# Performance work log

Measured on AMD Instinct MI355X. Metric: run time of the kernel, lower is better.

Reference implementation:

```python
import jax, jax.numpy as jnp
import numpy as np

INPUT_DIM = 1024
LATENT_DIM = 256
NUM_EMB = 8192
BATCH = 8192


def setup_inputs() -> dict:
    key = jax.random.key(0)
    ks = jax.random.split(key, 6)
    x = jax.random.normal(ks[0], (BATCH, INPUT_DIM), dtype=jnp.float32)
    # torch nn.Linear stores weight as [out, in]
    enc_w = jax.random.normal(ks[1], (LATENT_DIM, INPUT_DIM), dtype=jnp.float32) / np.sqrt(INPUT_DIM)
    enc_b = jnp.zeros((LATENT_DIM,), dtype=jnp.float32)
    # embeddings initialized uniform(-1/K, 1/K) as in the module
    emb = jax.random.uniform(ks[2], (NUM_EMB, LATENT_DIM), dtype=jnp.float32,
                             minval=-1.0 / NUM_EMB, maxval=1.0 / NUM_EMB)
    dec_w = jax.random.normal(ks[3], (INPUT_DIM, LATENT_DIM), dtype=jnp.float32) / np.sqrt(LATENT_DIM)
    dec_b = jnp.zeros((INPUT_DIM,), dtype=jnp.float32)
    return {"x": x, "enc_w": enc_w, "enc_b": enc_b, "emb": emb,
            "dec_w": dec_w, "dec_b": dec_b}


def reference(x, enc_w, enc_b, emb, dec_w, dec_b):
    # encoder: z = x @ W_e^T + b_e  -> [B, D]
    z = x @ enc_w.T + enc_b
    # cosine distance to codebook: d = 1 - <z, e> / (||z|| ||e||)  -> [B, K]
    z_norm = jnp.linalg.norm(z, axis=1, keepdims=True)          # [B, 1]
    e_norm = jnp.linalg.norm(emb, axis=1)                        # [K]
    d = 1.0 - (z @ emb.T) / (z_norm * e_norm)
    idx = jnp.argmin(d, axis=1)                                  # [B]
    # one-hot @ codebook == direct gather of nearest code vectors
    z_q = jnp.take(emb, idx, axis=0)                             # [B, D]
    # straight-through: decoder input z + stop_grad(z_q - z)
    dec_in = z + jax.lax.stop_gradient(z_q - z)
    x_recon = dec_in @ dec_w.T + dec_b
    return (x_recon, z, z_q, idx.astype(jnp.int32))
```

## Files before the change

### kernel.cpp

```cpp
#include <hip/hip_runtime.h>
#include <math.h>

#define BATCH   8192
#define IN_DIM  1024
#define LAT     256
#define NEMB    8192

#define TAU 3.5e-3f

#define RESC_R 16

#define CSPLIT 16

typedef _Float16 f16x8 __attribute__((ext_vector_type(8)));
typedef _Float16 f16x4 __attribute__((ext_vector_type(4)));
typedef float f32x16_t __attribute__((ext_vector_type(16)));

typedef __attribute__((address_space(1))) const unsigned int gu32_t;
typedef __attribute__((address_space(3))) unsigned int lu32_t;

__device__ __forceinline__ unsigned int ford(float x) {
  unsigned int u = __float_as_uint(x);
  return (u & 0x80000000u) ? ~u : (u | 0x80000000u);
}
__device__ __forceinline__ float funord(unsigned int t) {
  unsigned int u = (t & 0x80000000u) ? (t & 0x7FFFFFFFu) : ~t;
  return __uint_as_float(u);
}

__global__ __launch_bounds__(256) void emb_norms(
    const float* __restrict__ emb, float* __restrict__ inv_norm) {
  int row = blockIdx.x * 4 + (threadIdx.x >> 6);
  int lane = threadIdx.x & 63;
  const float* p = emb + (size_t)row * LAT;
  float s = 0.f;
#pragma unroll
  for (int t = 0; t < 4; ++t) {
    float v = p[lane + 64 * t];
    s += v * v;
  }
#pragma unroll
  for (int off = 32; off; off >>= 1) s += __shfl_xor(s, off);
  if (lane == 0) inv_norm[row] = 1.0f / sqrtf(s);
}

__global__ __launch_bounds__(256) void split16(
    const float* __restrict__ src, const float* __restrict__ inv_norm,
    _Float16* __restrict__ dst, size_t lo_off, int KD, int write_lo) {
  int gw = (blockIdx.x * 256 + threadIdx.x) >> 6;
  int l = threadIdx.x & 63;
  int tile = gw / KD, kb = gw % KD;
  int row = tile * 32 + (l & 31);
  int k = kb * 16 + (l >> 5) * 8;
  const float* p = src + (size_t)row * (KD * 16) + k;
  float scale = inv_norm ? inv_norm[row] : 1.0f;
  f16x8 h, lo;
#pragma unroll
  for (int j = 0; j < 8; ++j) {
    float v = p[j] * scale;
    _Float16 hh = (_Float16)v;
    h[j] = hh;
    lo[j] = (_Float16)(v - (float)hh);
  }
  size_t o = ((size_t)gw * 64 + l) * 8;
  *(f16x8*)(dst + o) = h;
  if (write_lo) *(f16x8*)(dst + lo_off + o) = lo;
}

__global__ __launch_bounds__(256) void gemm16_frag(
    const _Float16* __restrict__ Afrag, size_t a_lo_off,
    const _Float16* __restrict__ Bfrag, size_t b_lo_off,
    const float* __restrict__ bias, float* __restrict__ C, int N, int K) {
  __shared__ char lds[32768];
  const int tid = threadIdx.x;
  const int l = tid & 63;
  const int w = tid >> 6;
  const int mt = w & 1, nt = w >> 1;
  const int rb = blockIdx.y * 64, cb = blockIdx.x * 64;
  const int KD = K >> 4;

  f32x16_t acc = (f32x16_t)0.0f;

  for (int s = 0; s < (K >> 6); ++s) {
#pragma unroll
    for (int i = 0; i < 8; ++i) {
      int c = i * 4 + w;
      int isB = c >> 4;
      int cc = c & 15;
      int t32 = cc >> 3, prec = (cc >> 2) & 1, ks = cc & 3;
      int tile = ((isB ? cb : rb) >> 5) + t32;
      int kb = s * 4 + ks;
      const _Float16* base = isB ? Bfrag : Afrag;
      size_t lo = isB ? b_lo_off : a_lo_off;
      const _Float16* src =
          base + (size_t)prec * lo + ((size_t)(tile * KD + kb) * 64 + l) * 8;
      __builtin_amdgcn_global_load_lds((gu32_t*)src,
                                       (lu32_t*)(lds + (c << 10) + l * 16),
                                       16, 0, 0);
    }
    __syncthreads();
#pragma unroll
    for (int ks = 0; ks < 4; ++ks) {
      f16x8 ah = *(const f16x8*)(lds + ((mt * 8 + ks) << 10) + l * 16);
      f16x8 al = *(const f16x8*)(lds + ((mt * 8 + 4 + ks) << 10) + l * 16);
      f16x8 bh = *(const f16x8*)(lds + 16384 + ((nt * 8 + ks) << 10) + l * 16);
      f16x8 bl = *(const f16x8*)(lds + 16384 + ((nt * 8 + 4 + ks) << 10) + l * 16);
      acc = __builtin_amdgcn_mfma_f32_32x32x16_f16(ah, bh, acc, 0, 0, 0);
      acc = __builtin_amdgcn_mfma_f32_32x32x16_f16(ah, bl, acc, 0, 0, 0);
      acc = __builtin_amdgcn_mfma_f32_32x32x16_f16(al, bh, acc, 0, 0, 0);
    }
    __syncthreads();
  }

  int col = cb + nt * 32 + (l & 31);
  float bv = bias[col];
#pragma unroll
  for (int r = 0; r < 16; ++r) {
    int row = rb + mt * 32 + (r & 3) + 8 * (r >> 2) + 4 * (l >> 5);
    C[(size_t)row * N + col] = acc[r] + bv;
  }
}

__global__ __launch_bounds__(256) void gemm16(
    const float* __restrict__ A, const _Float16* __restrict__ Bfrag,
    size_t b_lo_off, const float* __restrict__ bias, float* __restrict__ C,
    int M, int N, int K) {
  __shared__ char lds[32768];
  const int tid = threadIdx.x;
  const int l = tid & 63;
  const int w = tid >> 6;
  const int mt = w & 1, nt = w >> 1;
  const int rb = blockIdx.y * 64, cb = blockIdx.x * 64;
  const int KD = K >> 4;

  f32x16_t acc = (f32x16_t)0.0f;

  for (int s = 0; s < (K >> 6); ++s) {
#pragma unroll
    for (int i = 0; i < 4; ++i) {
      int c = i * 4 + w;
      int bnt = c >> 3, prec = (c >> 2) & 1, ks = c & 3;
      int tile = (cb >> 5) + bnt, ksg = s * 4 + ks;
      const _Float16* src = Bfrag + (size_t)prec * b_lo_off +
                            ((size_t)(tile * KD + ksg) * 64 + l) * 8;
      __builtin_amdgcn_global_load_lds((gu32_t*)src,
                                       (lu32_t*)(lds + 16384 + (c << 10) + l * 16),
                                       16, 0, 0);
    }
#pragma unroll
    for (int t = 0; t < 4; ++t) {
      int flat = t * 256 + tid;
      int r = flat >> 4, c4 = flat & 15;
      float4 v = *(const float4*)&A[(size_t)(rb + r) * K + s * 64 + 4 * c4];
      int kk = 4 * c4;
      int ks = kk >> 4, j = kk & 7;
      int lane2 = (r & 31) + 32 * ((kk >> 3) & 1);
      int mtt = r >> 5;
      f16x4 hv, lv;
      float vv[4] = {v.x, v.y, v.z, v.w};
#pragma unroll
      for (int e = 0; e < 4; ++e) {
        _Float16 h = (_Float16)vv[e];
        hv[e] = h;
        lv[e] = (_Float16)(vv[e] - (float)h);
      }
      int base = ((mtt * 8 + ks) << 10) + lane2 * 16 + j * 2;
      *(f16x4*)(lds + base) = hv;
      *(f16x4*)(lds + base + 4096) = lv;
    }
    __syncthreads();
#pragma unroll
    for (int ks = 0; ks < 4; ++ks) {
      f16x8 ah = *(const f16x8*)(lds + ((mt * 8 + ks) << 10) + l * 16);
      f16x8 al = *(const f16x8*)(lds + ((mt * 8 + 4 + ks) << 10) + l * 16);
      f16x8 bh = *(const f16x8*)(lds + 16384 + ((nt * 8 + ks) << 10) + l * 16);
      f16x8 bl = *(const f16x8*)(lds + 16384 + ((nt * 8 + 4 + ks) << 10) + l * 16);
      acc = __builtin_amdgcn_mfma_f32_32x32x16_f16(ah, bh, acc, 0, 0, 0);
      acc = __builtin_amdgcn_mfma_f32_32x32x16_f16(ah, bl, acc, 0, 0, 0);
      acc = __builtin_amdgcn_mfma_f32_32x32x16_f16(al, bh, acc, 0, 0, 0);
    }
    __syncthreads();
  }

  int col = cb + nt * 32 + (l & 31);
  float bv = bias[col];
#pragma unroll
  for (int r = 0; r < 16; ++r) {
    int row = rb + mt * 32 + (r & 3) + 8 * (r >> 2) + 4 * (l >> 5);
    C[(size_t)row * N + col] = acc[r] + bv;
  }
}

__global__ __launch_bounds__(256) void score_mfma(
    const _Float16* __restrict__ zfrag, const _Float16* __restrict__ efrag,
    unsigned long long* __restrict__ cand1, unsigned int* __restrict__ cand2) {
  __shared__ char lds[32768];
  const int tid = threadIdx.x;
  const int l = tid & 63;
  const int w = tid >> 6;
  const int csplit = blockIdx.x;
  const int rowgrp = blockIdx.y;

  f16x8 a[16];
  {
    const _Float16* ab =
        zfrag + (((size_t)(rowgrp * 4 + w) * 16) * 64 + l) * 8;
#pragma unroll
    for (int kf = 0; kf < 16; ++kf)
      a[kf] = *(const f16x8*)(ab + (size_t)kf * 512);
  }

  float b1[16], b2[16];
  int i1[16];
#pragma unroll
  for (int r = 0; r < 16; ++r) {
    b1[r] = -INFINITY;
    b2[r] = -INFINITY;
    i1[r] = 0;
  }

  const char* esrc = (const char*)efrag + (size_t)csplit * 262144 + tid * 16;
  char* ldst = lds + tid * 16;
  const char* ldsr = lds + l * 16;

#pragma unroll
  for (int i = 0; i < 4; ++i)
    __builtin_amdgcn_global_load_lds((gu32_t*)(esrc + i * 4096),
                                     (lu32_t*)(ldst + i * 4096), 16, 0, 0);

#pragma unroll 1
  for (int p = 0; p < 16; ++p) {
    asm volatile("s_waitcnt vmcnt(0)" ::: "memory");
    __builtin_amdgcn_s_barrier();
    __builtin_amdgcn_sched_barrier(0);

    if (p < 15) {
      const char* sb = esrc + (size_t)(p + 1) * 16384;
      char* db = ldst + ((p + 1) & 1) * 16384;
#pragma unroll
      for (int i = 0; i < 4; ++i)
        __builtin_amdgcn_global_load_lds((gu32_t*)(sb + i * 4096),
                                         (lu32_t*)(db + i * 4096), 16, 0, 0);
    }

    const char* bb = ldsr + (p & 1) * 16384;
    f32x16_t acc0 = (f32x16_t)0.0f;
    f32x16_t acc1 = (f32x16_t)0.0f;
#pragma unroll
    for (int kb = 0; kb < 16; kb += 2) {
      f16x8 bh0 = *(const f16x8*)(bb + (kb << 10));
      f16x8 bh1 = *(const f16x8*)(bb + ((kb + 1) << 10));
      acc0 = __builtin_amdgcn_mfma_f32_32x32x16_f16(a[kb], bh0, acc0, 0, 0, 0);
      acc1 = __builtin_amdgcn_mfma_f32_32x32x16_f16(a[kb + 1], bh1, acc1, 0, 0, 0);
    }

    const int col = csplit * 512 + p * 32 + (l & 31);
#pragma unroll
    for (int r = 0; r < 16; ++r) {
      float v = acc0[r] + acc1[r];
      float nb2 = __builtin_amdgcn_fmed3f(v, b1[r], b2[r]);
      if (v > b1[r]) i1[r] = col;
      b1[r] = fmaxf(b1[r], v);
      b2[r] = nb2;
    }
  }

#pragma unroll
  for (int r = 0; r < 16; ++r) {
    float v1 = b1[r], v2 = b2[r];
    int vi = i1[r];
#pragma unroll
    for (int m = 1; m < 32; m <<= 1) {
      float o1 = __shfl_xor(v1, m);
      int oi = __shfl_xor(vi, m);
      float o2 = __shfl_xor(v2, m);
      float n2v = fmaxf(fminf(v1, o1), fmaxf(v2, o2));
      if (o1 > v1 || (o1 == v1 && oi < vi)) {
        v1 = o1;
        vi = oi;
      }
      v2 = n2v;
    }
    if ((l & 31) == 0) {
      int row = rowgrp * 128 + w * 32 + (r & 3) + 8 * (r >> 2) + 4 * (l >> 5);
      cand1[(size_t)row * CSPLIT + csplit] =
          ((unsigned long long)ford(v1) << 32) |
          (unsigned long long)(unsigned int)(NEMB - 1 - vi);
      cand2[(size_t)row * CSPLIT + csplit] = ford(v2);
    }
  }
}

__global__ __launch_bounds__(256) void finalize1(
    const unsigned long long* __restrict__ cand1,
    const unsigned int* __restrict__ cand2, int* __restrict__ idxi,
    unsigned int* __restrict__ flags, unsigned int* __restrict__ flag_count,
    unsigned int* __restrict__ flag_list) {
  int row = blockIdx.x * 256 + threadIdx.x;
  unsigned long long best = 0;
  unsigned int second = 0;
  int bslot = 0;
#pragma unroll
  for (int s = 0; s < CSPLIT; ++s) {
    unsigned long long v = cand1[(size_t)row * CSPLIT + s];
    unsigned int vs = (unsigned int)(v >> 32);
    if (v > best) {
      second = (unsigned int)(best >> 32);
      best = v;
      bslot = s;
    } else if (vs > second) {
      second = vs;
    }
  }
  unsigned int r2 = cand2[(size_t)row * CSPLIT + bslot];
  if (r2 > second) second = r2;
  float s1 = funord((unsigned int)(best >> 32));
  float s2 = funord(second);
  int idx = NEMB - 1 - (int)(best & 0xFFFFFFFFull);
  idxi[row] = idx;
  unsigned int fl = ((s1 - s2) < TAU) ? 1u : 0u;
  flags[row] = fl;
  if (fl) {
    unsigned int p = atomicAdd(flag_count, 1u);
    flag_list[p] = row;
  }
}

__global__ __launch_bounds__(256) void rescore(
    const float* __restrict__ z, const float* __restrict__ emb,
    const float* __restrict__ inv_norm,
    const unsigned int* __restrict__ flag_list,
    const unsigned int* __restrict__ flag_count,
    unsigned long long* __restrict__ packed_rescore) {
  __shared__ float z_s[2][292];
  __shared__ unsigned long long red[64];
  const int tid = threadIdx.x;
  const int l = tid & 63;
  const int w = tid >> 6;
  const int cl = l & 7;
  const int p = l >> 3;
  const int code = w * 8 + cl;
  const int cbase = blockIdx.x * 32;
  const unsigned int rc = blockIdx.y;

  unsigned int cnt = *flag_count;
  if (2 * rc >= cnt) return;

  float4 e4[8];
  const float* ebase = emb + (size_t)(cbase + code) * 256 + p * 32;
#pragma unroll
  for (int j = 0; j < 8; ++j) e4[j] = *(const float4*)&ebase[4 * j];
  const float inv = inv_norm[cbase + code];
  const unsigned int lowbits = (unsigned int)(NEMB - 1 - (cbase + code));

  for (unsigned int f = 2 * rc; f < cnt; f += 2 * RESC_R) {
    int row0 = (int)flag_list[f];
    int row1 = (f + 1 < cnt) ? (int)flag_list[f + 1] : row0;
    __syncthreads();
    if (tid < 128) {
      int half = tid >> 6, t = tid & 63;
      int k0 = t * 4;
      int addr = k0 + 4 * (k0 >> 5);
      const float* zp = z + (size_t)(half ? row1 : row0) * 256 + k0;
      *(float4*)&z_s[half][addr] = *(const float4*)zp;
    }
    __syncthreads();
    float a0 = 0.f, a1 = 0.f;
#pragma unroll
    for (int j = 0; j < 8; ++j) {
      float4 z0 = *(const float4*)&z_s[0][p * 36 + 4 * j];
      float4 z1 = *(const float4*)&z_s[1][p * 36 + 4 * j];
      a0 += e4[j].x * z0.x + e4[j].y * z0.y + e4[j].z * z0.z + e4[j].w * z0.w;
      a1 += e4[j].x * z1.x + e4[j].y * z1.y + e4[j].z * z1.z + e4[j].w * z1.w;
    }
#pragma unroll
    for (int m = 8; m < 64; m <<= 1) {
      a0 += __shfl_xor(a0, m);
      a1 += __shfl_xor(a1, m);
    }
    if (l < 8)
      red[w * 8 + cl] = ((unsigned long long)ford(a0 * inv) << 32) | lowbits;
    else if (l < 16)
      red[32 + w * 8 + cl] = ((unsigned long long)ford(a1 * inv) << 32) | lowbits;
    __syncthreads();
    if (w == 0) {
      unsigned long long v = red[l];
#pragma unroll
      for (int m = 1; m < 32; m <<= 1) {
        unsigned long long o = __shfl_xor(v, m);
        if (o > v) v = o;
      }
      if (l == 0) atomicMax(&packed_rescore[row0], v);
      if (l == 32) atomicMax(&packed_rescore[row1], v);
    }
  }
}

__global__ __launch_bounds__(256) void gather_split(
    const int* __restrict__ idxi, const unsigned int* __restrict__ flags,
    const unsigned long long* __restrict__ packed_rescore,
    const float* __restrict__ emb, float* __restrict__ zq,
    float* __restrict__ idx_out, _Float16* __restrict__ zqfrag,
    size_t lo_off, int use_frag) {
  __shared__ float zrow[32][260];
  __shared__ int idxs[32];
  const int tid = threadIdx.x;
  const int tile = blockIdx.x;
  if (tid < 32) {
    int row = tile * 32 + tid;
    int idx = idxi[row];
    if (flags[row]) idx = NEMB - 1 - (int)(packed_rescore[row] & 0xFFFFFFFFull);
    idxs[tid] = idx;
    idx_out[row] = (float)idx;
  }
  __syncthreads();
#pragma unroll
  for (int t = 0; t < 8; ++t) {
    int flat = t * 256 + tid;
    int r = flat >> 6, c4 = flat & 63;
    float4 v = *(const float4*)&emb[(size_t)idxs[r] * 256 + 4 * c4];
    *(float4*)&zrow[r][4 * c4] = v;
    *(float4*)&zq[(size_t)(tile * 32 + r) * 256 + 4 * c4] = v;
  }
  if (use_frag) {
    __syncthreads();
#pragma unroll
    for (int t = 0; t < 4; ++t) {
      int flat = t * 256 + tid;
      int fb = flat >> 6, fl = flat & 63;
      int r = fl & 31, k0 = fb * 16 + (fl >> 5) * 8;
      float4 v0 = *(const float4*)&zrow[r][k0];
      float4 v1 = *(const float4*)&zrow[r][k0 + 4];
      float vv[8] = {v0.x, v0.y, v0.z, v0.w, v1.x, v1.y, v1.z, v1.w};
      f16x8 hv, lv;
#pragma unroll
      for (int j = 0; j < 8; ++j) {
        _Float16 h = (_Float16)vv[j];
        hv[j] = h;
        lv[j] = (_Float16)(vv[j] - (float)h);
      }
      size_t g = ((size_t)(tile * 16 + fb) * 64 + fl) * 8;
      *(f16x8*)(zqfrag + g) = hv;
      *(f16x8*)(zqfrag + lo_off + g) = lv;
    }
  }
}

extern "C" void kernel_launch(void* const* d_in, const int* in_sizes, int n_in,
                              void* d_out, int out_size, void* d_ws,
                              size_t ws_size, hipStream_t stream) {
  (void)in_sizes; (void)n_in; (void)out_size;
  const float* x     = (const float*)d_in[0];
  const float* enc_w = (const float*)d_in[1];
  const float* enc_b = (const float*)d_in[2];
  const float* emb   = (const float*)d_in[3];
  const float* dec_w = (const float*)d_in[4];
  const float* dec_b = (const float*)d_in[5];

  float* out     = (float*)d_out;
  float* x_recon = out;
  float* z_out   = x_recon + (size_t)BATCH * IN_DIM;
  float* zq_out  = z_out + (size_t)BATCH * LAT;
  float* idx_out = zq_out + (size_t)BATCH * LAT;

  char* ws = (char*)d_ws;
  float* inv_norm = (float*)ws;
  unsigned int* flags = (unsigned int*)(ws + 32768);
  int* idxi = (int*)(ws + 65536);
  unsigned int* flag_count = (unsigned int*)(ws + 98304);
  unsigned long long* packed_rescore =
      (unsigned long long*)(ws + 98432);
  unsigned int* flag_list = (unsigned int*)(ws + 163968);
  _Float16* wfrag  = (_Float16*)(ws + 1048576);
  _Float16* dwfrag = (_Float16*)(ws + 2097152);
  _Float16* efrag  = (_Float16*)(ws + 3145728);
  _Float16* zfrag  = (_Float16*)(ws + 7340032);
  unsigned long long* cand1 = (unsigned long long*)(ws + 11534336);
  unsigned int* cand2 = (unsigned int*)(ws + 12582912);
  _Float16* zqfrag = (_Float16*)(ws + 15728640);
  _Float16* xfrag  = (_Float16*)(ws + 24117248);

  const bool has_zq = ws_size >= 24117248ull;
  const bool has_x  = ws_size >= 57671680ull;

  hipMemsetAsync(ws + 98304, 0, 128 + 65536, stream);

  emb_norms<<<NEMB / 4, 256, 0, stream>>>(emb, inv_norm);
  split16<<<128, 256, 0, stream>>>(enc_w, (const float*)nullptr, wfrag,
                                   (size_t)LAT * IN_DIM, IN_DIM / 16, 1);
  split16<<<128, 256, 0, stream>>>(dec_w, (const float*)nullptr, dwfrag,
                                   (size_t)IN_DIM * LAT, LAT / 16, 1);
  split16<<<1024, 256, 0, stream>>>(emb, inv_norm, efrag, 0, LAT / 16, 0);

  if (has_x) {
    split16<<<4096, 256, 0, stream>>>(x, (const float*)nullptr, xfrag,
                                      (size_t)BATCH * IN_DIM, IN_DIM / 16, 1);
    gemm16_frag<<<dim3(LAT / 64, BATCH / 64), 256, 0, stream>>>(
        xfrag, (size_t)BATCH * IN_DIM, wfrag, (size_t)LAT * IN_DIM, enc_b,
        z_out, LAT, IN_DIM);
  } else {
    gemm16<<<dim3(LAT / 64, BATCH / 64), 256, 0, stream>>>(
        x, wfrag, (size_t)LAT * IN_DIM, enc_b, z_out, BATCH, LAT, IN_DIM);
  }

  split16<<<1024, 256, 0, stream>>>(z_out, (const float*)nullptr, zfrag,
                                    (size_t)BATCH * LAT, LAT / 16, 0);

  score_mfma<<<dim3(CSPLIT, 64), 256, 0, stream>>>(zfrag, efrag, cand1, cand2);

  finalize1<<<32, 256, 0, stream>>>(cand1, cand2, idxi, flags, flag_count,
                                    flag_list);
  rescore<<<dim3(256, RESC_R), 256, 0, stream>>>(
      z_out, emb, inv_norm, flag_list, flag_count, packed_rescore);

  gather_split<<<BATCH / 32, 256, 0, stream>>>(
      idxi, flags, packed_rescore, emb, zq_out, idx_out,
      has_zq ? zqfrag : (_Float16*)nullptr, (size_t)BATCH * LAT,
      has_zq ? 1 : 0);

  if (has_zq) {
    gemm16_frag<<<dim3(IN_DIM / 64, BATCH / 64), 256, 0, stream>>>(
        zqfrag, (size_t)BATCH * LAT, dwfrag, (size_t)IN_DIM * LAT, dec_b,
        x_recon, IN_DIM, LAT);
  } else {
    gemm16<<<dim3(IN_DIM / 64, BATCH / 64), 256, 0, stream>>>(
        zq_out, dwfrag, (size_t)IN_DIM * LAT, dec_b, x_recon, BATCH, IN_DIM,
        LAT);
  }
}
```

Baseline: 267.2 us.

## Load codebook fragments directly from global memory in score kernel, dropping LDS staging

The score kernel no longer stages codebook tiles through a double-buffered LDS ring filled by global_load_lds with barriers. Each wave now reads its B fragments straight from global memory (relying on L2 and cache for reuse across the 4 waves) and uses a single accumulator chain instead of two interleaved ones. This removes per-tile barriers, the LDS footprint and the waitcnt stalls, but it loses explicit prefetch overlap and the two-accumulator MFMA interleaving, and it multiplies global traffic by the wave count.

```diff
diff --git a/kernel.cpp b/kernel.cpp
--- a/kernel.cpp
+++ b/kernel.cpp
@@ -194,7 +194,6 @@
 __global__ __launch_bounds__(256) void score_mfma(
     const _Float16* __restrict__ zfrag, const _Float16* __restrict__ efrag,
     unsigned long long* __restrict__ cand1, unsigned int* __restrict__ cand2) {
-  __shared__ char lds[32768];
   const int tid = threadIdx.x;
   const int l = tid & 63;
   const int w = tid >> 6;
@@ -219,45 +218,22 @@
     i1[r] = 0;
   }
 
-  const char* esrc = (const char*)efrag + (size_t)csplit * 262144 + tid * 16;
-  char* ldst = lds + tid * 16;
-  const char* ldsr = lds + l * 16;
-
-#pragma unroll
-  for (int i = 0; i < 4; ++i)
-    __builtin_amdgcn_global_load_lds((gu32_t*)(esrc + i * 4096),
-                                     (lu32_t*)(ldst + i * 4096), 16, 0, 0);
+  const _Float16* eb = efrag + (size_t)csplit * 131072 + (size_t)l * 8;
 
 #pragma unroll 1
-  for (int p = 0; p < 16; ++p) {
-    asm volatile("s_waitcnt vmcnt(0)" ::: "memory");
-    __builtin_amdgcn_s_barrier();
-    __builtin_amdgcn_sched_barrier(0);
-
-    if (p < 15) {
-      const char* sb = esrc + (size_t)(p + 1) * 16384;
-      char* db = ldst + ((p + 1) & 1) * 16384;
-#pragma unroll
-      for (int i = 0; i < 4; ++i)
-        __builtin_amdgcn_global_load_lds((gu32_t*)(sb + i * 4096),
-                                         (lu32_t*)(db + i * 4096), 16, 0, 0);
-    }
-
-    const char* bb = ldsr + (p & 1) * 16384;
-    f32x16_t acc0 = (f32x16_t)0.0f;
-    f32x16_t acc1 = (f32x16_t)0.0f;
-#pragma unroll
-    for (int kb = 0; kb < 16; kb += 2) {
-      f16x8 bh0 = *(const f16x8*)(bb + (kb << 10));
-      f16x8 bh1 = *(const f16x8*)(bb + ((kb + 1) << 10));
-      acc0 = __builtin_amdgcn_mfma_f32_32x32x16_f16(a[kb], bh0, acc0, 0, 0, 0);
-      acc1 = __builtin_amdgcn_mfma_f32_32x32x16_f16(a[kb + 1], bh1, acc1, 0, 0, 0);
-    }
-
-    const int col = csplit * 512 + p * 32 + (l & 31);
+  for (int t = 0; t < 16; ++t) {
+    const _Float16* bt = eb + (size_t)t * 8192;
+    f32x16_t acc = (f32x16_t)0.0f;
+#pragma unroll
+    for (int kb = 0; kb < 16; ++kb) {
+      f16x8 bh = *(const f16x8*)(bt + kb * 512);
+      acc = __builtin_amdgcn_mfma_f32_32x32x16_f16(a[kb], bh, acc, 0, 0, 0);
+    }
+
+    const int col = csplit * 512 + t * 32 + (l & 31);
 #pragma unroll
     for (int r = 0; r < 16; ++r) {
-      float v = acc0[r] + acc1[r];
+      float v = acc[r];
       float nb2 = __builtin_amdgcn_fmed3f(v, b1[r], b2[r]);
       if (v > b1[r]) i1[r] = col;
       b1[r] = fmaxf(b1[r], v);
```

Result: slower. 323.7 us (+21.2%).

## Fuse codebook gather and fp16 split into decoder GEMM; merge prep kernels

Applied to the files above, without the earlier changes.

Removes the gather_split kernel and the zq fragment buffer. The decoder GEMM now resolves each row's index, gathers the code vectors from emb, splits them into hi/lo fp16 directly into LDS, and writes zq and idx from the blockIdx.x==0 blocks. Embedding norm and fragment conversion are fused into one emb_prep kernel, and the two weight splits are merged into a single launch. This cuts launches and a global round trip for zq fragments, but each of the 16 column blocks repeats the emb gather and split for its rows, and the uncoalesced gather now sits inside the GEMM loop.

```diff
diff --git a/kernel.cpp b/kernel.cpp
--- a/kernel.cpp
+++ b/kernel.cpp
@@ -28,36 +28,61 @@
   return __uint_as_float(u);
 }
 
-__global__ __launch_bounds__(256) void emb_norms(
-    const float* __restrict__ emb, float* __restrict__ inv_norm) {
-  int row = blockIdx.x * 4 + (threadIdx.x >> 6);
-  int lane = threadIdx.x & 63;
-  const float* p = emb + (size_t)row * LAT;
-  float s = 0.f;
-#pragma unroll
-  for (int t = 0; t < 4; ++t) {
-    float v = p[lane + 64 * t];
-    s += v * v;
-  }
-#pragma unroll
-  for (int off = 32; off; off >>= 1) s += __shfl_xor(s, off);
-  if (lane == 0) inv_norm[row] = 1.0f / sqrtf(s);
-}
-
-__global__ __launch_bounds__(256) void split16(
-    const float* __restrict__ src, const float* __restrict__ inv_norm,
-    _Float16* __restrict__ dst, size_t lo_off, int KD, int write_lo) {
-  int gw = (blockIdx.x * 256 + threadIdx.x) >> 6;
-  int l = threadIdx.x & 63;
+__global__ __launch_bounds__(256) void emb_prep(
+    const float* __restrict__ emb, float* __restrict__ inv_norm,
+    _Float16* __restrict__ efrag) {
+  __shared__ float s_inv[32];
+  const int tid = threadIdx.x;
+  const int l = tid & 63;
+  const int w = tid >> 6;
+  const int tile = blockIdx.x;
+
+  {
+    int row = tid >> 3, part = tid & 7;
+    const float* p = emb + (size_t)(tile * 32 + row) * 256 + part * 32;
+    float s = 0.f;
+#pragma unroll
+    for (int j = 0; j < 8; ++j) {
+      float4 v = *(const float4*)&p[4 * j];
+      s += v.x * v.x + v.y * v.y + v.z * v.z + v.w * v.w;
+    }
+    s += __shfl_xor(s, 1);
+    s += __shfl_xor(s, 2);
+    s += __shfl_xor(s, 4);
+    if (part == 0) {
+      float iv = 1.0f / sqrtf(s);
+      s_inv[row] = iv;
+      inv_norm[tile * 32 + row] = iv;
+    }
+  }
+  __syncthreads();
+
+#pragma unroll
+  for (int q = 0; q < 4; ++q) {
+    int kb = w * 4 + q;
+    int row = l & 31;
+    int k = kb * 16 + (l >> 5) * 8;
+    const float* p = emb + (size_t)(tile * 32 + row) * 256 + k;
+    float sc = s_inv[row];
+    f16x8 h;
+#pragma unroll
+    for (int j = 0; j < 8; ++j) h[j] = (_Float16)(p[j] * sc);
+    size_t o = ((size_t)(tile * 16 + kb) * 64 + l) * 8;
+    *(f16x8*)(efrag + o) = h;
+  }
+}
+
+__device__ __forceinline__ void split_body(
+    const float* __restrict__ src, _Float16* __restrict__ dst, size_t lo_off,
+    int KD, int write_lo, int gw, int l) {
   int tile = gw / KD, kb = gw % KD;
   int row = tile * 32 + (l & 31);
   int k = kb * 16 + (l >> 5) * 8;
   const float* p = src + (size_t)row * (KD * 16) + k;
-  float scale = inv_norm ? inv_norm[row] : 1.0f;
   f16x8 h, lo;
 #pragma unroll
   for (int j = 0; j < 8; ++j) {
-    float v = p[j] * scale;
+    float v = p[j];
     _Float16 hh = (_Float16)v;
     h[j] = hh;
     lo[j] = (_Float16)(v - (float)hh);
@@ -65,6 +90,27 @@
   size_t o = ((size_t)gw * 64 + l) * 8;
   *(f16x8*)(dst + o) = h;
   if (write_lo) *(f16x8*)(dst + lo_off + o) = lo;
+}
+
+__global__ __launch_bounds__(256) void split16(
+    const float* __restrict__ src, _Float16* __restrict__ dst, size_t lo_off,
+    int KD, int write_lo) {
+  int gw = (blockIdx.x * 256 + threadIdx.x) >> 6;
+  split_body(src, dst, lo_off, KD, write_lo, gw, threadIdx.x & 63);
+}
+
+__global__ __launch_bounds__(256) void split_weights(
+    const float* __restrict__ enc_w, _Float16* __restrict__ wfrag,
+    const float* __restrict__ dec_w, _Float16* __restrict__ dwfrag) {
+  int b = blockIdx.x;
+  int l = threadIdx.x & 63;
+  if (b < 128) {
+    int gw = (b * 256 + threadIdx.x) >> 6;
+    split_body(enc_w, wfrag, (size_t)LAT * IN_DIM, IN_DIM / 16, 1, gw, l);
+  } else {
+    int gw = ((b - 128) * 256 + threadIdx.x) >> 6;
+    split_body(dec_w, dwfrag, (size_t)IN_DIM * LAT, LAT / 16, 1, gw, l);
+  }
 }
 
 __global__ __launch_bounds__(256) void gemm16_frag(
@@ -188,6 +234,90 @@
   for (int r = 0; r < 16; ++r) {
     int row = rb + mt * 32 + (r & 3) + 8 * (r >> 2) + 4 * (l >> 5);
     C[(size_t)row * N + col] = acc[r] + bv;
+  }
+}
+
+__global__ __launch_bounds__(256) void gemm16_dec(
+    const int* __restrict__ idxi, const unsigned int* __restrict__ flags,
+    const unsigned long long* __restrict__ packed_rescore,
+    const float* __restrict__ emb, const _Float16* __restrict__ Bfrag,
+    size_t b_lo_off, const float* __restrict__ bias, float* __restrict__ C,
+    float* __restrict__ zq, float* __restrict__ idx_out) {
+  __shared__ char lds[32768];
+  __shared__ int idxs[64];
+  const int tid = threadIdx.x;
+  const int l = tid & 63;
+  const int w = tid >> 6;
+  const int mt = w & 1, nt = w >> 1;
+  const int rb = blockIdx.y * 64, cb = blockIdx.x * 64;
+  const int KD = 16;
+
+  if (tid < 64) {
+    int row = rb + tid;
+    int idx = idxi[row];
+    if (flags[row]) idx = NEMB - 1 - (int)(packed_rescore[row] & 0xFFFFFFFFull);
+    idxs[tid] = idx;
+    if (blockIdx.x == 0) idx_out[row] = (float)idx;
+  }
+  __syncthreads();
+
+  f32x16_t acc = (f32x16_t)0.0f;
+
+  for (int s = 0; s < 4; ++s) {
+#pragma unroll
+    for (int i = 0; i < 4; ++i) {
+      int c = i * 4 + w;
+      int bnt = c >> 3, prec = (c >> 2) & 1, ks = c & 3;
+      int tile = (cb >> 5) + bnt, ksg = s * 4 + ks;
+      const _Float16* src = Bfrag + (size_t)prec * b_lo_off +
+                            ((size_t)(tile * KD + ksg) * 64 + l) * 8;
+      __builtin_amdgcn_global_load_lds((gu32_t*)src,
+                                       (lu32_t*)(lds + 16384 + (c << 10) + l * 16),
+                                       16, 0, 0);
+    }
+#pragma unroll
+    for (int t = 0; t < 4; ++t) {
+      int flat = t * 256 + tid;
+      int r = flat >> 4, c4 = flat & 15;
+      float4 v = *(const float4*)&emb[(size_t)idxs[r] * 256 + s * 64 + 4 * c4];
+      if (blockIdx.x == 0)
+        *(float4*)&zq[(size_t)(rb + r) * 256 + s * 64 + 4 * c4] = v;
+      int kk = 4 * c4;
+      int ks = kk >> 4, j = kk & 7;
+      int lane2 = (r & 31) + 32 * ((kk >> 3) & 1);
+      int mtt = r >> 5;
+      f16x4 hv, lv;
+      float vv[4] = {v.x, v.y, v.z, v.w};
+#pragma unroll
+      for (int e = 0; e < 4; ++e) {
+        _Float16 h = (_Float16)vv[e];
+        hv[e] = h;
+        lv[e] = (_Float16)(vv[e] - (float)h);
+      }
+      int base = ((mtt * 8 + ks) << 10) + lane2 * 16 + j * 2;
+      *(f16x4*)(lds + base) = hv;
+      *(f16x4*)(lds + base + 4096) = lv;
+    }
+    __syncthreads();
+#pragma unroll
+    for (int ks = 0; ks < 4; ++ks) {
+      f16x8 ah = *(const f16x8*)(lds + ((mt * 8 + ks) << 10) + l * 16);
+      f16x8 al = *(const f16x8*)(lds + ((mt * 8 + 4 + ks) << 10) + l * 16);
+      f16x8 bh = *(const f16x8*)(lds + 16384 + ((nt * 8 + ks) << 10) + l * 16);
+      f16x8 bl = *(const f16x8*)(lds + 16384 + ((nt * 8 + 4 + ks) << 10) + l * 16);
+      acc = __builtin_amdgcn_mfma_f32_32x32x16_f16(ah, bh, acc, 0, 0, 0);
+      acc = __builtin_amdgcn_mfma_f32_32x32x16_f16(ah, bl, acc, 0, 0, 0);
+      acc = __builtin_amdgcn_mfma_f32_32x32x16_f16(al, bh, acc, 0, 0, 0);
+    }
+    __syncthreads();
+  }
+
+  int col = cb + nt * 32 + (l & 31);
+  float bv = bias[col];
+#pragma unroll
+  for (int r = 0; r < 16; ++r) {
+    int row = rb + mt * 32 + (r & 3) + 8 * (r >> 2) + 4 * (l >> 5);
+    C[(size_t)row * IN_DIM + col] = acc[r] + bv;
   }
 }
 
@@ -396,56 +526,6 @@
   }
 }
 
-__global__ __launch_bounds__(256) void gather_split(
-    const int* __restrict__ idxi, const unsigned int* __restrict__ flags,
-    const unsigned long long* __restrict__ packed_rescore,
-    const float* __restrict__ emb, float* __restrict__ zq,
-    float* __restrict__ idx_out, _Float16* __restrict__ zqfrag,
-    size_t lo_off, int use_frag) {
-  __shared__ float zrow[32][260];
-  __shared__ int idxs[32];
-  const int tid = threadIdx.x;
-  const int tile = blockIdx.x;
-  if (tid < 32) {
-    int row = tile * 32 + tid;
-    int idx = idxi[row];
-    if (flags[row]) idx = NEMB - 1 - (int)(packed_rescore[row] & 0xFFFFFFFFull);
-    idxs[tid] = idx;
-    idx_out[row] = (float)idx;
-  }
-  __syncthreads();
-#pragma unroll
-  for (int t = 0; t < 8; ++t) {
-    int flat = t * 256 + tid;
-    int r = flat >> 6, c4 = flat & 63;
-    float4 v = *(const float4*)&emb[(size_t)idxs[r] * 256 + 4 * c4];
-    *(float4*)&zrow[r][4 * c4] = v;
-    *(float4*)&zq[(size_t)(tile * 32 + r) * 256 + 4 * c4] = v;
-  }
-  if (use_frag) {
-    __syncthreads();
-#pragma unroll
-    for (int t = 0; t < 4; ++t) {
-      int flat = t * 256 + tid;
-      int fb = flat >> 6, fl = flat & 63;
-      int r = fl & 31, k0 = fb * 16 + (fl >> 5) * 8;
-      float4 v0 = *(const float4*)&zrow[r][k0];
-      float4 v1 = *(const float4*)&zrow[r][k0 + 4];
-      float vv[8] = {v0.x, v0.y, v0.z, v0.w, v1.x, v1.y, v1.z, v1.w};
-      f16x8 hv, lv;
-#pragma unroll
-      for (int j = 0; j < 8; ++j) {
-        _Float16 h = (_Float16)vv[j];
-        hv[j] = h;
-        lv[j] = (_Float16)(vv[j] - (float)h);
-      }
-      size_t g = ((size_t)(tile * 16 + fb) * 64 + fl) * 8;
-      *(f16x8*)(zqfrag + g) = hv;
-      *(f16x8*)(zqfrag + lo_off + g) = lv;
-    }
-  }
-}
-
 extern "C" void kernel_launch(void* const* d_in, const int* in_sizes, int n_in,
                               void* d_out, int out_size, void* d_ws,
                               size_t ws_size, hipStream_t stream) {
@@ -477,24 +557,18 @@
   _Float16* zfrag  = (_Float16*)(ws + 7340032);
   unsigned long long* cand1 = (unsigned long long*)(ws + 11534336);
   unsigned int* cand2 = (unsigned int*)(ws + 12582912);
-  _Float16* zqfrag = (_Float16*)(ws + 15728640);
   _Float16* xfrag  = (_Float16*)(ws + 24117248);
 
-  const bool has_zq = ws_size >= 24117248ull;
-  const bool has_x  = ws_size >= 57671680ull;
+  const bool has_x = ws_size >= 57671680ull;
 
   hipMemsetAsync(ws + 98304, 0, 128 + 65536, stream);
 
-  emb_norms<<<NEMB / 4, 256, 0, stream>>>(emb, inv_norm);
-  split16<<<128, 256, 0, stream>>>(enc_w, (const float*)nullptr, wfrag,
-                                   (size_t)LAT * IN_DIM, IN_DIM / 16, 1);
-  split16<<<128, 256, 0, stream>>>(dec_w, (const float*)nullptr, dwfrag,
-                                   (size_t)IN_DIM * LAT, LAT / 16, 1);
-  split16<<<1024, 256, 0, stream>>>(emb, inv_norm, efrag, 0, LAT / 16, 0);
+  emb_prep<<<NEMB / 32, 256, 0, stream>>>(emb, inv_norm, efrag);
+  split_weights<<<256, 256, 0, stream>>>(enc_w, wfrag, dec_w, dwfrag);
 
   if (has_x) {
-    split16<<<4096, 256, 0, stream>>>(x, (const float*)nullptr, xfrag,
-                                      (size_t)BATCH * IN_DIM, IN_DIM / 16, 1);
+    split16<<<4096, 256, 0, stream>>>(x, xfrag, (size_t)BATCH * IN_DIM,
+                                      IN_DIM / 16, 1);
     gemm16_frag<<<dim3(LAT / 64, BATCH / 64), 256, 0, stream>>>(
         xfrag, (size_t)BATCH * IN_DIM, wfrag, (size_t)LAT * IN_DIM, enc_b,
         z_out, LAT, IN_DIM);
@@ -503,8 +577,8 @@
         x, wfrag, (size_t)LAT * IN_DIM, enc_b, z_out, BATCH, LAT, IN_DIM);
   }
 
-  split16<<<1024, 256, 0, stream>>>(z_out, (const float*)nullptr, zfrag,
-                                    (size_t)BATCH * LAT, LAT / 16, 0);
+  split16<<<1024, 256, 0, stream>>>(z_out, zfrag, (size_t)BATCH * LAT,
+                                    LAT / 16, 0);
 
   score_mfma<<<dim3(CSPLIT, 64), 256, 0, stream>>>(zfrag, efrag, cand1, cand2);
 
@@ -513,18 +587,7 @@
   rescore<<<dim3(256, RESC_R), 256, 0, stream>>>(
       z_out, emb, inv_norm, flag_list, flag_count, packed_rescore);
 
-  gather_split<<<BATCH / 32, 256, 0, stream>>>(
-      idxi, flags, packed_rescore, emb, zq_out, idx_out,
-      has_zq ? zqfrag : (_Float16*)nullptr, (size_t)BATCH * LAT,
-      has_zq ? 1 : 0);
-
-  if (has_zq) {
-    gemm16_frag<<<dim3(IN_DIM / 64, BATCH / 64), 256, 0, stream>>>(
-        zqfrag, (size_t)BATCH * LAT, dwfrag, (size_t)IN_DIM * LAT, dec_b,
-        x_recon, IN_DIM, LAT);
-  } else {
-    gemm16<<<dim3(IN_DIM / 64, BATCH / 64), 256, 0, stream>>>(
-        zq_out, dwfrag, (size_t)IN_DIM * LAT, dec_b, x_recon, BATCH, IN_DIM,
-        LAT);
-  }
-}
+  gemm16_dec<<<dim3(IN_DIM / 64, BATCH / 64), 256, 0, stream>>>(
+      idxi, flags, packed_rescore, emb, dwfrag, (size_t)IN_DIM * LAT, dec_b,
+      x_recon, zq_out, idx_out);
+}
```

Measured after the change: 261.8 us. 2.0% less time.
